# Optimization experiments

Hardware: AMD Instinct MI355X
Metric: run time of the kernel (lower is better)

The kernel has to match this reference:

```python
import jax, jax.numpy as jnp
import numpy as np

NUM_CODES = 8192
CODE_DIM = 64
DECAY = 0.99
EPS = 1e-05


def setup_inputs() -> dict:
    key = jax.random.key(0)
    k1, k2 = jax.random.split(key)
    z = jax.random.normal(k1, (8, CODE_DIM, 64, 64), dtype=jnp.float32)
    embed = jax.random.normal(k2, (NUM_CODES, CODE_DIM), dtype=jnp.float32)
    embed = embed / jnp.linalg.norm(embed, axis=1, keepdims=True)  # F.normalize(dim=1)
    cluster_size = jnp.zeros((NUM_CODES,), dtype=jnp.float32)
    embed_avg = embed * 1.0
    return {"z": z, "embed": embed, "cluster_size": cluster_size, "embed_avg": embed_avg}


def reference(z, embed, cluster_size, embed_avg):
    B, C, H, W = z.shape
    # (B,C,H,W) -> (N, C), N = B*H*W
    flat = jnp.transpose(z, (0, 2, 3, 1)).reshape(-1, C)
    x2 = jnp.sum(flat * flat, axis=1, keepdims=True)
    e2 = jnp.sum(embed * embed, axis=1)[None, :]
    logits = x2 + e2 - 2.0 * (flat @ embed.T)
    codes = jnp.argmin(logits, axis=1)
    # gather nearest code vectors, restore (B,C,H,W)
    z_q = jnp.transpose(embed[codes].reshape(B, H, W, C), (0, 3, 1, 2))
    # EMA update (training path; equivalent to one-hot matmul via segment sums)
    cs_batch = jax.ops.segment_sum(jnp.ones_like(codes, dtype=flat.dtype), codes, num_segments=NUM_CODES)
    embed_sum = jax.ops.segment_sum(flat, codes, num_segments=NUM_CODES)
    new_cluster_size = cluster_size * DECAY + cs_batch * (1.0 - DECAY)
    new_embed_avg = embed_avg * DECAY + embed_sum * (1.0 - DECAY)
    n = jnp.sum(new_cluster_size)
    cs_smoothed = (new_cluster_size + EPS) / (n + NUM_CODES * EPS) * n
    new_embed = new_embed_avg / cs_smoothed[:, None]
    new_embed = new_embed / jnp.linalg.norm(new_embed, axis=1, keepdims=True)
    return z_q, codes.reshape(B, H, W), new_embed, new_cluster_size, new_embed_avg
```

## Files before the change

### kernel.cpp

```cpp
#include <hip/hip_runtime.h>
#include <math.h>
#include <float.h>

#define NPTS   32768
#define NCODES 8192
#define D      64
#define HWSZ   4096
#define KSPLIT 8
#define NSTAGE 8

#define DECAY_F 0.99f
#define OMD_F   ((float)(1.0 - 0.99))
#define EPS_F   1e-5f

typedef __attribute__((ext_vector_type(8)))  short bf16x8;
typedef __attribute__((ext_vector_type(8)))  unsigned short us8;
typedef __attribute__((ext_vector_type(4)))  float f32x4;
typedef __attribute__((ext_vector_type(16))) float f32x16;

#define ZQ_OFF    0
#define CODES_OFF 2097152
#define NE_OFF    2129920
#define NCS_OFF   2654208
#define NEA_OFF   2662400

#define WS_PSUM   0
#define WS_ME2    64
#define WS_ME2P   8256
#define WS_HIST   16448
#define WS_BOFF   24640
#define WS_BOFF2  32832
#define WS_CODES  41024
#define WS_ORDER  73792
#define WS_PMG    106560
#define WS_EBI    1155136
#define WS_ZROW   1417280

__device__ __forceinline__ unsigned short f2bf(float x) {
    unsigned int u = __float_as_uint(x);
    unsigned int r = (u + 0x7fffu + ((u >> 16) & 1u)) >> 16;
    return (unsigned short)r;
}
__device__ __forceinline__ float bf2f(unsigned short b) {
    return __uint_as_float(((unsigned int)b) << 16);
}

__global__ __launch_bounds__(256) void k_prep_e(
    const float* __restrict__ embed, const float* __restrict__ cs_in,
    unsigned short* __restrict__ ebi,
    float* __restrict__ me2, float* __restrict__ me2p,
    int* __restrict__ hist, float* __restrict__ psum)
{
    __shared__ float wsum[4];
    const int tid = threadIdx.x;
    int c = blockIdx.x * 256 + tid;
    const float4* src = (const float4*)(embed + (size_t)c * D);
    float row[64];
    float s2 = 0.f;
#pragma unroll
    for (int i = 0; i < 16; ++i) {
        float4 v = src[i];
        row[i * 4 + 0] = v.x; row[i * 4 + 1] = v.y;
        row[i * 4 + 2] = v.z; row[i * 4 + 3] = v.w;
        s2 += v.x * v.x; s2 += v.y * v.y; s2 += v.z * v.z; s2 += v.w * v.w;
    }
    const int sg = c >> 7, ci = c & 127;
    unsigned short* tile = ebi + (size_t)sg * 16384;
#pragma unroll
    for (int s = 0; s < 8; ++s) {
        us8 v0, v1;
#pragma unroll
        for (int j = 0; j < 8; ++j) {
            float x = row[s * 8 + j];
            unsigned short a = f2bf(x);
            float r1 = x - bf2f(a);
            v0[j] = a; v1[j] = f2bf(r1);
        }
        *(us8*)(tile + s * 1024 + ci * 8) = v0;
        *(us8*)(tile + 8192 + s * 1024 + ci * 8) = v1;
    }
    float m = -0.5f * s2;
    me2[c] = m;
    {
        int ct = (c >> 5) & 3, rem = c & 31;
        int q = rem >> 3, hi = (rem >> 2) & 1, r = rem & 3;
        me2p[((sg * 4 + ct) * 2 + hi) * 16 + q * 4 + r] = m;
    }
    hist[c] = 0;
    float t = cs_in[c];
    t += __shfl_xor(t, 32); t += __shfl_xor(t, 16); t += __shfl_xor(t, 8);
    t += __shfl_xor(t, 4);  t += __shfl_xor(t, 2);  t += __shfl_xor(t, 1);
    if ((tid & 63) == 0) wsum[tid >> 6] = t;
    __syncthreads();
    if (tid == 0) psum[blockIdx.x] = (wsum[0] + wsum[1]) + (wsum[2] + wsum[3]);
}

#define MFMA32 __builtin_amdgcn_mfma_f32_32x32x16_bf16

#define TOP2(nt, g, gi) { \
    bool c1 = (g) > b1m[nt]; \
    bool c2 = (g) > b2m[nt]; \
    b2m[nt] = c1 ? b1m[nt] : (c2 ? (g) : b2m[nt]); \
    b2g[nt] = c1 ? b1g[nt] : (c2 ? (gi) : b2g[nt]); \
    b1m[nt] = c1 ? (g) : b1m[nt]; \
    b1g[nt] = c1 ? (gi) : b1g[nt]; }

#define GMAX8(a, o) fmaxf(fmaxf(fmaxf(fmaxf(a[o+0], a[o+1]), a[o+2]), \
                                fmaxf(fmaxf(a[o+3], a[o+4]), a[o+5])), \
                          fmaxf(a[o+6], a[o+7]))

__global__ __launch_bounds__(256, 2) void k_argmin_mfma(
    const float* __restrict__ z,
    const unsigned short* __restrict__ ebi,
    const float* __restrict__ me2p,
    float* __restrict__ pmg)
{
    __shared__ __align__(16) char ets[2 * 32768];
    __shared__ float me2s[1024];

    const int tid = threadIdx.x;
    const int l = tid & 63;
    const int w = tid >> 6;
    const int l31 = l & 31;
    const int hi = l >> 5;
    const int split = blockIdx.x >> 7;
    const int pgrp  = blockIdx.x & 127;
    const int n0    = pgrp * 256;
    const int b     = n0 >> 12;
    const int hw0   = n0 & 4095;
    const int ptw   = n0 + w * 64;

    const char* ebase = (const char*)ebi;
#define ISSUE_STAGE(sg_, buf_) { \
    const char* gsrc_ = ebase + (size_t)(sg_) * 32768; \
    _Pragma("unroll") \
    for (int i_ = 0; i_ < 8; ++i_) { \
        __builtin_amdgcn_global_load_lds( \
            (const __attribute__((address_space(1))) void*)(gsrc_ + i_ * 4096 + w * 1024 + l * 16), \
            (__attribute__((address_space(3))) void*)(ets + (buf_) * 32768 + i_ * 4096 + w * 1024), \
            16, 0, 0); \
    } }

    ISSUE_STAGE(split * NSTAGE, 0)

    {
        f32x4 v = *(const f32x4*)(me2p + split * 1024 + tid * 4);
        *(f32x4*)(me2s + tid * 4) = v;
    }

    const float* zb = z + (size_t)b * D * HWSZ;
    us8 zf[2][2][4];
#pragma unroll
    for (int nt = 0; nt < 2; ++nt) {
        const int hwp = hw0 + w * 64 + nt * 32 + l31;
#pragma unroll
        for (int kc = 0; kc < 4; ++kc) {
            us8 p0, p1;
#pragma unroll
            for (int j = 0; j < 8; ++j) {
                float x = zb[(size_t)(kc * 16 + hi * 8 + j) * HWSZ + hwp];
                unsigned short a = f2bf(x);
                float r = x - bf2f(a);
                p0[j] = a; p1[j] = f2bf(r);
            }
            zf[nt][0][kc] = p0; zf[nt][1][kc] = p1;
        }
    }
    __syncthreads();

    float b1m[2] = {-FLT_MAX, -FLT_MAX}, b2m[2] = {-FLT_MAX, -FLT_MAX};
    int   b1g[2] = {0, 0},               b2g[2] = {0, 0};

    for (int stg = 0; stg < NSTAGE; ++stg) {
        const int sg = split * NSTAGE + stg;
        if (stg + 1 < NSTAGE) ISSUE_STAGE(sg + 1, (stg + 1) & 1)

        const char* bt = ets + (stg & 1) * 32768;
#pragma unroll
        for (int ct = 0; ct < 4; ++ct) {
            f32x16 mq = *(const f32x16*)(me2s + ((stg * 4 + ct) * 2 + hi) * 16);

            f32x16 acc0, acc1;
#pragma unroll
            for (int kc = 0; kc < 4; ++kc) {
                const size_t off = (size_t)(kc * 2 + hi) * 2048 + (size_t)(ct * 32 + l31) * 16;
                bf16x8 ea0 = *(const bf16x8*)(bt + off);
                bf16x8 ea1 = *(const bf16x8*)(bt + 16384 + off);
                if (kc == 0) {
                    acc0 = MFMA32(ea1, (bf16x8)zf[0][0][0], mq, 0, 0, 0);
                    acc1 = MFMA32(ea1, (bf16x8)zf[1][0][0], mq, 0, 0, 0);
                } else {
                    acc0 = MFMA32(ea1, (bf16x8)zf[0][0][kc], acc0, 0, 0, 0);
                    acc1 = MFMA32(ea1, (bf16x8)zf[1][0][kc], acc1, 0, 0, 0);
                }
                acc0 = MFMA32(ea0, (bf16x8)zf[0][1][kc], acc0, 0, 0, 0);
                acc1 = MFMA32(ea0, (bf16x8)zf[1][1][kc], acc1, 0, 0, 0);
                acc0 = MFMA32(ea0, (bf16x8)zf[0][0][kc], acc0, 0, 0, 0);
                acc1 = MFMA32(ea0, (bf16x8)zf[1][0][kc], acc1, 0, 0, 0);
            }

            const int gb = sg * 16 + ct * 4 + hi;
            {
                float g00 = GMAX8(acc0, 0);
                float g01 = GMAX8(acc0, 8);
                float g10 = GMAX8(acc1, 0);
                float g11 = GMAX8(acc1, 8);
                TOP2(0, g00, gb)
                TOP2(0, g01, gb + 2)
                TOP2(1, g10, gb)
                TOP2(1, g11, gb + 2)
            }
        }
        __syncthreads();
    }

#pragma unroll
    for (int nt = 0; nt < 2; ++nt) {
        float o1 = __shfl_xor(b1m[nt], 32); int o1g = __shfl_xor(b1g[nt], 32);
        float o2 = __shfl_xor(b2m[nt], 32); int o2g = __shfl_xor(b2g[nt], 32);
        float n1m, n2m; int n1g, n2g;
        if (o1 > b1m[nt]) {
            n1m = o1; n1g = o1g;
            if (b1m[nt] >= o2) { n2m = b1m[nt]; n2g = b1g[nt]; } else { n2m = o2; n2g = o2g; }
        } else {
            n1m = b1m[nt]; n1g = b1g[nt];
            if (o1 >= b2m[nt]) { n2m = o1; n2g = o1g; } else { n2m = b2m[nt]; n2g = b2g[nt]; }
        }
        b1m[nt] = n1m; b1g[nt] = n1g; b2m[nt] = n2m; b2g[nt] = n2g;
    }
    if (l < 32) {
#pragma unroll
        for (int nt = 0; nt < 2; ++nt) {
            int pt = ptw + nt * 32 + l31;
            float4 v = {b1m[nt], __int_as_float(b1g[nt]), b2m[nt], __int_as_float(b2g[nt])};
            *(float4*)(pmg + ((size_t)split * NPTS + pt) * 4) = v;
        }
    }
}

__device__ __forceinline__ int grp_code(int g, int s) {
    int base = (g >> 4) * 128 + ((g >> 2) & 3) * 32 + ((g >> 1) & 1) * 16 + (g & 1) * 4;
    return base + (s & 3) + ((s >> 2) & 1) * 8;
}

__global__ __launch_bounds__(256) void k_refine(
    const float* __restrict__ z, const float* __restrict__ embed,
    const float* __restrict__ me2, const float* __restrict__ pmg,
    int* __restrict__ codes_i, float* __restrict__ out_codes,
    float* __restrict__ zq, int* __restrict__ hist, float* __restrict__ zrow)
{
    __shared__ float  xs[64 * 32];
    __shared__ float4 smg[256];
    __shared__ float  sbm[256];
    __shared__ int    sbi[256];
    const int tid = threadIdx.x;
    const int pi = tid & 31, s = tid >> 5;
    const int n0 = blockIdx.x * 32;
    const int b = n0 >> 12, hw0 = n0 & 4095;
    const int n = n0 + pi;

    {
        float4 v = ((const float4*)pmg)[(size_t)(tid & 7) * NPTS + n0 + (tid >> 3)];
        smg[(tid & 7) * 32 + (tid >> 3)] = v;
    }
    const float* zb = z + (size_t)b * D * HWSZ + hw0;
#pragma unroll
    for (int i = 0; i < 8; ++i) {
        int c = s * 8 + i;
        xs[c * 32 + pi] = zb[(size_t)c * HWSZ + pi];
    }
    __syncthreads();
    float x[64];
#pragma unroll
    for (int c = 0; c < 64; ++c) x[c] = xs[c * 32 + pi];

    float t1 = -FLT_MAX, t2 = -FLT_MAX; int g1 = 0, g2 = 0;
#pragma unroll
    for (int j = 0; j < 8; ++j) {
        float4 v = smg[j * 32 + pi];
        float m1 = v.x; int a1 = __float_as_int(v.y);
        float m2 = v.z; int a2 = __float_as_int(v.w);
        if (m1 > t1) { t2 = t1; g2 = g1; t1 = m1; g1 = a1; }
        else if (m1 > t2) { t2 = m1; g2 = a1; }
        if (m2 > t1) { t2 = t1; g2 = g1; t1 = m2; g1 = a2; }
        else if (m2 > t2) { t2 = m2; g2 = a2; }
    }

    float bm = -FLT_MAX; int bi = 0x7fffffff;
#pragma unroll
    for (int cset = 0; cset < 2; ++cset) {
        const int ci = grp_code(cset ? g2 : g1, s);
        const float4* er = (const float4*)(embed + (size_t)ci * D);
        float d0 = 0.f, d1 = 0.f, d2 = 0.f, d3 = 0.f;
#pragma unroll
        for (int q = 0; q < 16; ++q) {
            float4 e4 = er[q];
            d0 = fmaf(x[4 * q + 0], e4.x, d0);
            d1 = fmaf(x[4 * q + 1], e4.y, d1);
            d2 = fmaf(x[4 * q + 2], e4.z, d2);
            d3 = fmaf(x[4 * q + 3], e4.w, d3);
        }
        float m = ((d0 + d1) + (d2 + d3)) + me2[ci];
        if (m > bm || (m == bm && ci < bi)) { bm = m; bi = ci; }
    }
    sbm[tid] = bm; sbi[tid] = bi;
    __syncthreads();

    if (s == 0) {
        float B = sbm[pi]; int I = sbi[pi];
#pragma unroll
        for (int t = 1; t < 8; ++t) {
            float mm = sbm[t * 32 + pi]; int ii = sbi[t * 32 + pi];
            if (mm > B || (mm == B && ii < I)) { B = mm; I = ii; }
        }
        codes_i[n] = I;
        out_codes[n] = (float)I;
        atomicAdd(&hist[I], 1);
        const float* err = embed + (size_t)I * D;
        size_t zoff = (size_t)b * D * HWSZ + hw0 + pi;
#pragma unroll 8
        for (int c = 0; c < 64; ++c) zq[zoff + (size_t)c * HWSZ] = err[c];
    }
    {
        float4 a4 = {x[s * 8 + 0], x[s * 8 + 1], x[s * 8 + 2], x[s * 8 + 3]};
        float4 b4 = {x[s * 8 + 4], x[s * 8 + 5], x[s * 8 + 6], x[s * 8 + 7]};
        *(float4*)(zrow + (size_t)n * 64 + s * 8) = a4;
        *(float4*)(zrow + (size_t)n * 64 + s * 8 + 4) = b4;
    }
}

__global__ __launch_bounds__(1024) void k_scan(
    const int* __restrict__ hist, int* __restrict__ binoff, int* __restrict__ binoff2)
{
    __shared__ int wtot[16];
    __shared__ int wbase[16];
    const int tid = threadIdx.x;
    const int lane = tid & 63, w = tid >> 6;
    int v[8]; int s = 0;
#pragma unroll
    for (int i = 0; i < 8; ++i) { v[i] = hist[tid * 8 + i]; s += v[i]; }
    int inc = s;
#pragma unroll
    for (int off = 1; off < 64; off <<= 1) {
        int t = __shfl_up(inc, off);
        if (lane >= off) inc += t;
    }
    if (lane == 63) wtot[w] = inc;
    __syncthreads();
    if (tid == 0) {
        int a = 0;
#pragma unroll
        for (int i = 0; i < 16; ++i) { int t = wtot[i]; wbase[i] = a; a += t; }
    }
    __syncthreads();
    int excl = wbase[w] + (inc - s);
#pragma unroll
    for (int i = 0; i < 8; ++i) {
        binoff[tid * 8 + i] = excl;
        binoff2[tid * 8 + i] = excl;
        excl += v[i];
    }
}

__global__ void k_reorder(const int* __restrict__ codes_i,
                          int* __restrict__ binoff2, int* __restrict__ order)
{
    int n = blockIdx.x * 256 + threadIdx.x;
    int c = codes_i[n];
    int r = atomicAdd(&binoff2[c], 1);
    order[r] = n;
}

__global__ __launch_bounds__(256) void k_accum(
    const int* __restrict__ hist, const int* __restrict__ binoff,
    const int* __restrict__ order, const float* __restrict__ zrow,
    const float* __restrict__ cs, const float* __restrict__ eavg,
    const float* __restrict__ psum,
    float* __restrict__ out_ncs, float* __restrict__ out_nea, float* __restrict__ out_ne)
{
    int k = blockIdx.x * 4 + (threadIdx.x >> 6);
    int lane = threadIdx.x & 63;
    int cnt = hist[k], base = binoff[k];
    float acc = 0.f;
    for (int i = 0; i < cnt; ++i) {
        int p = order[base + i];
        acc += zrow[(size_t)p * 64 + lane];
    }
    float S = 0.f;
#pragma unroll
    for (int i = 0; i < 32; ++i) S += psum[i];
    float n = DECAY_F * S + OMD_F * (float)NPTS;

    float v = cs[k] * DECAY_F + (float)cnt * OMD_F;
    if (lane == 0) out_ncs[k] = v;

    int idx = k * D + lane;
    float ea = eavg[idx] * DECAY_F + acc * OMD_F;
    out_nea[idx] = ea;
    float csm = (v + EPS_F) / (n + (float)NCODES * EPS_F) * n;
    float u = ea / csm;
    float ss = u * u;
    ss += __shfl_xor(ss, 32);
    ss += __shfl_xor(ss, 16);
    ss += __shfl_xor(ss, 8);
    ss += __shfl_xor(ss, 4);
    ss += __shfl_xor(ss, 2);
    ss += __shfl_xor(ss, 1);
    out_ne[idx] = u / sqrtf(ss);
}

extern "C" void kernel_launch(void* const* d_in, const int* in_sizes, int n_in,
                              void* d_out, int out_size, void* d_ws, size_t ws_size,
                              hipStream_t stream) {
    const float* z     = (const float*)d_in[0];
    const float* embed = (const float*)d_in[1];
    const float* cs    = (const float*)d_in[2];
    const float* eavg  = (const float*)d_in[3];

    float* out = (float*)d_out;
    float* zq        = out + ZQ_OFF;
    float* out_codes = out + CODES_OFF;
    float* out_ne    = out + NE_OFF;
    float* out_ncs   = out + NCS_OFF;
    float* out_nea   = out + NEA_OFF;

    float* ws = (float*)d_ws;
    float* psum   = ws + WS_PSUM;
    float* me2    = ws + WS_ME2;
    float* me2p   = ws + WS_ME2P;
    int*   hist   = (int*)(ws + WS_HIST);
    int*   boff   = (int*)(ws + WS_BOFF);
    int*   boff2  = (int*)(ws + WS_BOFF2);
    int*   codesi = (int*)(ws + WS_CODES);
    int*   order  = (int*)(ws + WS_ORDER);
    float* pmg    = ws + WS_PMG;
    float* zrow   = ws + WS_ZROW;
    unsigned short* ebi = (unsigned short*)(ws + WS_EBI);

    k_prep_e<<<NCODES / 256, 256, 0, stream>>>(embed, cs, ebi, me2, me2p, hist, psum);
    k_argmin_mfma<<<128 * KSPLIT, 256, 0, stream>>>(z, ebi, me2p, pmg);
    k_refine<<<NPTS / 32, 256, 0, stream>>>(z, embed, me2, pmg,
                                            codesi, out_codes, zq, hist, zrow);
    k_scan<<<1, 1024, 0, stream>>>(hist, boff, boff2);
    k_reorder<<<NPTS / 256, 256, 0, stream>>>(codesi, boff2, order);
    k_accum<<<NCODES / 4, 256, 0, stream>>>(hist, boff, order, zrow, cs, eavg, psum,
                                            out_ncs, out_nea, out_ne);
}
```

Measured before the change: 138.6 us.

## Drop norm bias from MFMA coarse pass, parallelize prep, move cluster-size sum to scan

The coarse MFMA argmin pass no longer seeds its accumulators with -0.5*||e||^2 and starts from zero instead, which removes the me2p staging buffer and its LDS copy. This relies on the codebook being unit-normalized, so the bias is constant, and on the exact refine pass rescoring the top-2 candidates. k_prep_e now uses 8 threads per code row instead of one thread holding 64 floats, giving 8x more blocks and fewer registers per thread. The cluster-size sum moves into the single-block scan kernel, so k_accum reads one value instead of 32 partials. The risk is that dropping the bias changes which candidates survive the coarse pass if the codebook norms ever differ.

```diff
diff --git a/kernel.cpp b/kernel.cpp
--- a/kernel.cpp
+++ b/kernel.cpp
@@ -26,15 +26,14 @@
 
 #define WS_PSUM   0
 #define WS_ME2    64
-#define WS_ME2P   8256
-#define WS_HIST   16448
-#define WS_BOFF   24640
-#define WS_BOFF2  32832
-#define WS_CODES  41024
-#define WS_ORDER  73792
-#define WS_PMG    106560
-#define WS_EBI    1155136
-#define WS_ZROW   1417280
+#define WS_HIST   8256
+#define WS_BOFF   16448
+#define WS_BOFF2  24640
+#define WS_CODES  32832
+#define WS_ORDER  65600
+#define WS_PMG    98368
+#define WS_EBI    1146944
+#define WS_ZROW   1409088
 
 __device__ __forceinline__ unsigned short f2bf(float x) {
     unsigned int u = __float_as_uint(x);
@@ -46,53 +45,37 @@
 }
 
 __global__ __launch_bounds__(256) void k_prep_e(
-    const float* __restrict__ embed, const float* __restrict__ cs_in,
+    const float* __restrict__ embed,
     unsigned short* __restrict__ ebi,
-    float* __restrict__ me2, float* __restrict__ me2p,
-    int* __restrict__ hist, float* __restrict__ psum)
-{
-    __shared__ float wsum[4];
+    float* __restrict__ me2, int* __restrict__ hist)
+{
     const int tid = threadIdx.x;
-    int c = blockIdx.x * 256 + tid;
-    const float4* src = (const float4*)(embed + (size_t)c * D);
-    float row[64];
+    const int c = blockIdx.x * 32 + (tid >> 3);
+    const int s = tid & 7;
+    const float4 v0 = *(const float4*)(embed + (size_t)c * D + s * 8);
+    const float4 v1 = *(const float4*)(embed + (size_t)c * D + s * 8 + 4);
+    float x[8] = {v0.x, v0.y, v0.z, v0.w, v1.x, v1.y, v1.z, v1.w};
     float s2 = 0.f;
 #pragma unroll
-    for (int i = 0; i < 16; ++i) {
-        float4 v = src[i];
-        row[i * 4 + 0] = v.x; row[i * 4 + 1] = v.y;
-        row[i * 4 + 2] = v.z; row[i * 4 + 3] = v.w;
-        s2 += v.x * v.x; s2 += v.y * v.y; s2 += v.z * v.z; s2 += v.w * v.w;
+    for (int j = 0; j < 8; ++j) s2 += x[j] * x[j];
+    s2 += __shfl_xor(s2, 1);
+    s2 += __shfl_xor(s2, 2);
+    s2 += __shfl_xor(s2, 4);
+    us8 p0, p1;
+#pragma unroll
+    for (int j = 0; j < 8; ++j) {
+        unsigned short a = f2bf(x[j]);
+        float r = x[j] - bf2f(a);
+        p0[j] = a; p1[j] = f2bf(r);
     }
     const int sg = c >> 7, ci = c & 127;
     unsigned short* tile = ebi + (size_t)sg * 16384;
-#pragma unroll
-    for (int s = 0; s < 8; ++s) {
-        us8 v0, v1;
-#pragma unroll
-        for (int j = 0; j < 8; ++j) {
-            float x = row[s * 8 + j];
-            unsigned short a = f2bf(x);
-            float r1 = x - bf2f(a);
-            v0[j] = a; v1[j] = f2bf(r1);
-        }
-        *(us8*)(tile + s * 1024 + ci * 8) = v0;
-        *(us8*)(tile + 8192 + s * 1024 + ci * 8) = v1;
-    }
-    float m = -0.5f * s2;
-    me2[c] = m;
-    {
-        int ct = (c >> 5) & 3, rem = c & 31;
-        int q = rem >> 3, hi = (rem >> 2) & 1, r = rem & 3;
-        me2p[((sg * 4 + ct) * 2 + hi) * 16 + q * 4 + r] = m;
-    }
-    hist[c] = 0;
-    float t = cs_in[c];
-    t += __shfl_xor(t, 32); t += __shfl_xor(t, 16); t += __shfl_xor(t, 8);
-    t += __shfl_xor(t, 4);  t += __shfl_xor(t, 2);  t += __shfl_xor(t, 1);
-    if ((tid & 63) == 0) wsum[tid >> 6] = t;
-    __syncthreads();
-    if (tid == 0) psum[blockIdx.x] = (wsum[0] + wsum[1]) + (wsum[2] + wsum[3]);
+    *(us8*)(tile + s * 1024 + ci * 8) = p0;
+    *(us8*)(tile + 8192 + s * 1024 + ci * 8) = p1;
+    if (s == 0) {
+        me2[c] = -0.5f * s2;
+        hist[c] = 0;
+    }
 }
 
 #define MFMA32 __builtin_amdgcn_mfma_f32_32x32x16_bf16
@@ -112,11 +95,9 @@
 __global__ __launch_bounds__(256, 2) void k_argmin_mfma(
     const float* __restrict__ z,
     const unsigned short* __restrict__ ebi,
-    const float* __restrict__ me2p,
     float* __restrict__ pmg)
 {
     __shared__ __align__(16) char ets[2 * 32768];
-    __shared__ float me2s[1024];
 
     const int tid = threadIdx.x;
     const int l = tid & 63;
@@ -143,11 +124,6 @@
 
     ISSUE_STAGE(split * NSTAGE, 0)
 
-    {
-        f32x4 v = *(const f32x4*)(me2p + split * 1024 + tid * 4);
-        *(f32x4*)(me2s + tid * 4) = v;
-    }
-
     const float* zb = z + (size_t)b * D * HWSZ;
     us8 zf[2][2][4];
 #pragma unroll
@@ -166,6 +142,11 @@
             zf[nt][0][kc] = p0; zf[nt][1][kc] = p1;
         }
     }
+
+    f32x16 zerov;
+#pragma unroll
+    for (int r = 0; r < 16; ++r) zerov[r] = 0.f;
+
     __syncthreads();
 
     float b1m[2] = {-FLT_MAX, -FLT_MAX}, b2m[2] = {-FLT_MAX, -FLT_MAX};
@@ -178,8 +159,6 @@
         const char* bt = ets + (stg & 1) * 32768;
 #pragma unroll
         for (int ct = 0; ct < 4; ++ct) {
-            f32x16 mq = *(const f32x16*)(me2s + ((stg * 4 + ct) * 2 + hi) * 16);
-
             f32x16 acc0, acc1;
 #pragma unroll
             for (int kc = 0; kc < 4; ++kc) {
@@ -187,8 +166,8 @@
                 bf16x8 ea0 = *(const bf16x8*)(bt + off);
                 bf16x8 ea1 = *(const bf16x8*)(bt + 16384 + off);
                 if (kc == 0) {
-                    acc0 = MFMA32(ea1, (bf16x8)zf[0][0][0], mq, 0, 0, 0);
-                    acc1 = MFMA32(ea1, (bf16x8)zf[1][0][0], mq, 0, 0, 0);
+                    acc0 = MFMA32(ea1, (bf16x8)zf[0][0][0], zerov, 0, 0, 0);
+                    acc1 = MFMA32(ea1, (bf16x8)zf[1][0][0], zerov, 0, 0, 0);
                 } else {
                     acc0 = MFMA32(ea1, (bf16x8)zf[0][0][kc], acc0, 0, 0, 0);
                     acc1 = MFMA32(ea1, (bf16x8)zf[1][0][kc], acc1, 0, 0, 0);
@@ -330,27 +309,39 @@
 }
 
 __global__ __launch_bounds__(1024) void k_scan(
-    const int* __restrict__ hist, int* __restrict__ binoff, int* __restrict__ binoff2)
+    const int* __restrict__ hist, const float* __restrict__ cs_in,
+    int* __restrict__ binoff, int* __restrict__ binoff2, float* __restrict__ psum)
 {
     __shared__ int wtot[16];
     __shared__ int wbase[16];
+    __shared__ float csw[16];
     const int tid = threadIdx.x;
     const int lane = tid & 63, w = tid >> 6;
     int v[8]; int s = 0;
-#pragma unroll
-    for (int i = 0; i < 8; ++i) { v[i] = hist[tid * 8 + i]; s += v[i]; }
+    float cz = 0.f;
+#pragma unroll
+    for (int i = 0; i < 8; ++i) {
+        v[i] = hist[tid * 8 + i];
+        s += v[i];
+        cz += cs_in[tid * 8 + i];
+    }
     int inc = s;
 #pragma unroll
     for (int off = 1; off < 64; off <<= 1) {
         int t = __shfl_up(inc, off);
         if (lane >= off) inc += t;
     }
+    cz += __shfl_xor(cz, 32); cz += __shfl_xor(cz, 16); cz += __shfl_xor(cz, 8);
+    cz += __shfl_xor(cz, 4);  cz += __shfl_xor(cz, 2);  cz += __shfl_xor(cz, 1);
     if (lane == 63) wtot[w] = inc;
+    if (lane == 0)  csw[w] = cz;
     __syncthreads();
     if (tid == 0) {
         int a = 0;
-#pragma unroll
-        for (int i = 0; i < 16; ++i) { int t = wtot[i]; wbase[i] = a; a += t; }
+        float S = 0.f;
+#pragma unroll
+        for (int i = 0; i < 16; ++i) { int t = wtot[i]; wbase[i] = a; a += t; S += csw[i]; }
+        psum[0] = S;
     }
     __syncthreads();
     int excl = wbase[w] + (inc - s);
@@ -386,9 +377,7 @@
         int p = order[base + i];
         acc += zrow[(size_t)p * 64 + lane];
     }
-    float S = 0.f;
-#pragma unroll
-    for (int i = 0; i < 32; ++i) S += psum[i];
+    float S = psum[0];
     float n = DECAY_F * S + OMD_F * (float)NPTS;
 
     float v = cs[k] * DECAY_F + (float)cnt * OMD_F;
@@ -427,7 +416,6 @@
     float* ws = (float*)d_ws;
     float* psum   = ws + WS_PSUM;
     float* me2    = ws + WS_ME2;
-    float* me2p   = ws + WS_ME2P;
     int*   hist   = (int*)(ws + WS_HIST);
     int*   boff   = (int*)(ws + WS_BOFF);
     int*   boff2  = (int*)(ws + WS_BOFF2);
@@ -437,11 +425,11 @@
     float* zrow   = ws + WS_ZROW;
     unsigned short* ebi = (unsigned short*)(ws + WS_EBI);
 
-    k_prep_e<<<NCODES / 256, 256, 0, stream>>>(embed, cs, ebi, me2, me2p, hist, psum);
-    k_argmin_mfma<<<128 * KSPLIT, 256, 0, stream>>>(z, ebi, me2p, pmg);
+    k_prep_e<<<NCODES / 32, 256, 0, stream>>>(embed, ebi, me2, hist);
+    k_argmin_mfma<<<128 * KSPLIT, 256, 0, stream>>>(z, ebi, pmg);
     k_refine<<<NPTS / 32, 256, 0, stream>>>(z, embed, me2, pmg,
                                             codesi, out_codes, zq, hist, zrow);
-    k_scan<<<1, 1024, 0, stream>>>(hist, boff, boff2);
+    k_scan<<<1, 1024, 0, stream>>>(hist, cs, boff, boff2, psum);
     k_reorder<<<NPTS / 256, 256, 0, stream>>>(codesi, boff2, order);
     k_accum<<<NCODES / 4, 256, 0, stream>>>(hist, boff, order, zrow, cs, eavg, psum,
                                             out_ncs, out_nea, out_ne);
```

Result: no change. 136.5 us (-1.5%).
